# Optimization experiments

Measured on AMD Instinct MI355X. Metric: run time of the kernel, lower is better.

## Reference

```python
import jax, jax.numpy as jnp
import numpy as np

N_NODES = 50000
N_EDGES = 800000
DIM_FEAT = 96
INFO_DIM = 32
DIM_EMB = 160
CONV_OUT = DIM_EMB - INFO_DIM  # 128
NUM_LAYERS = 3
NUM_GRAPHS = 500
DIM_TARGET = 10


def setup_inputs() -> dict:
    key = jax.random.key(0)
    ks = jax.random.split(key, 20)
    inp = {
        'x': jax.random.normal(ks[0], (N_NODES, DIM_FEAT), dtype=jnp.float32),
        'edge_index': jax.random.randint(ks[1], (2, N_EDGES), 0, N_NODES, dtype=jnp.int32),
        'batch': jnp.sort(jax.random.randint(ks[2], (N_NODES,), 0, NUM_GRAPHS, dtype=jnp.int32)),
        'struc_info': jax.random.normal(ks[3], (NUM_GRAPHS, INFO_DIM), dtype=jnp.float32),
    }
    # SAGEConv params per layer: lin_l (on aggregated neighbors, with bias), lin_r (on root, no bias)
    in_dims = [DIM_FEAT + INFO_DIM, DIM_EMB, DIM_EMB]
    k = 4
    for i, din in enumerate(in_dims):
        s = 1.0 / np.sqrt(din)
        inp[f'Wl{i}'] = jax.random.uniform(ks[k], (din, CONV_OUT), jnp.float32, -s, s); k += 1
        inp[f'Wr{i}'] = jax.random.uniform(ks[k], (din, CONV_OUT), jnp.float32, -s, s); k += 1
        inp[f'b{i}'] = jax.random.uniform(ks[k], (CONV_OUT,), jnp.float32, -s, s); k += 1
    s1 = 1.0 / np.sqrt(NUM_LAYERS * CONV_OUT)
    inp['Wfc1'] = jax.random.uniform(ks[k], (NUM_LAYERS * CONV_OUT, DIM_EMB), jnp.float32, -s1, s1); k += 1
    inp['bfc1'] = jax.random.uniform(ks[k], (DIM_EMB,), jnp.float32, -s1, s1); k += 1
    s2 = 1.0 / np.sqrt(DIM_EMB)
    inp['Wfc2'] = jax.random.uniform(ks[k], (DIM_EMB, DIM_TARGET), jnp.float32, -s2, s2); k += 1
    inp['bfc2'] = jax.random.uniform(ks[k], (DIM_TARGET,), jnp.float32, -s2, s2)
    return inp


def _sage_conv(h, src, dst, Wl, Wr, b, n_nodes):
    # PyG SAGEConv (mean aggr): out = lin_l(mean_{j in N(i)} x_j) + lin_r(x_i)
    agg = jax.ops.segment_sum(h[src], dst, num_segments=n_nodes)       # [N, D]
    deg = jax.ops.segment_sum(jnp.ones_like(dst, dtype=h.dtype), dst, num_segments=n_nodes)
    mean = agg / jnp.maximum(deg, 1.0)[:, None]
    return mean @ Wl + b + h @ Wr


def reference(x, edge_index, batch, struc_info, Wl0, Wr0, b0, Wl1, Wr1, b1, Wl2, Wr2, b2, Wfc1, bfc1, Wfc2, bfc2):
    n_nodes = x.shape[0]
    src, dst = edge_index[0], edge_index[1]
    info = struc_info[batch]                         # [N, info_dim] repeated per node
    params = [(Wl0, Wr0, b0), (Wl1, Wr1, b1), (Wl2, Wr2, b2)]
    h = x
    outs = []
    for (Wl, Wr, b) in params:
        h = _sage_conv(jnp.concatenate([h, info], axis=1), src, dst, Wl, Wr, b, n_nodes)
        outs.append(h)
    hcat = jnp.concatenate(outs, axis=1)             # [N, num_layers*conv_out]
    g = jax.ops.segment_max(hcat, batch, num_segments=struc_info.shape[0])  # global max pool
    z = jax.nn.relu(g @ Wfc1 + bfc1)
    return z @ Wfc2 + bfc2
```

## Files before the change

### kernel.cpp

```cpp
#include <hip/hip_runtime.h>
#include <hip/hip_bf16.h>
#include <float.h>

#define NN 50000
#define NE 800000
#define DF 96
#define DI 32
#define CO 128
#define NG 500
#define HC 384
#define F1I 384
#define F1O 160
#define F2O 10
#define CAPLOG 7

typedef unsigned int  u32;
typedef unsigned short u16;
typedef short bf16x8 __attribute__((ext_vector_type(8)));
typedef float f32x4  __attribute__((ext_vector_type(4)));

__device__ __forceinline__ u16 f2b(float f) {
    __hip_bfloat16 h = __float2bfloat16(f);
    return *reinterpret_cast<u16*>(&h);
}
__device__ __forceinline__ float b2f(u16 u) {
    return __uint_as_float(((u32)u) << 16);
}
__device__ __forceinline__ float blo(u32 u) { return __uint_as_float(u << 16); }
__device__ __forceinline__ float bhi(u32 u) { return __uint_as_float(u & 0xffff0000u); }

#define PB_CNT    196
#define PB_STARTS 196
#define PB_CAST   4688
#define PB_WT0    96
#define PB_WT1    128
#define PB_WT2    128
#define PB_INFO   500
#define PREP_GRID (PB_CNT + PB_STARTS + PB_CAST + PB_WT0 + PB_WT1 + PB_WT2 + 3 * PB_INFO)

__global__ __launch_bounds__(256) void k_prep(
        const float* __restrict__ x, const int* __restrict__ batch, const float* __restrict__ info,
        const float* __restrict__ Wl0, const float* __restrict__ Wr0, const float* __restrict__ b0,
        const float* __restrict__ Wl1, const float* __restrict__ Wr1, const float* __restrict__ b1,
        const float* __restrict__ Wl2, const float* __restrict__ Wr2, const float* __restrict__ b2,
        int* __restrict__ cnt, int* __restrict__ start, u16* __restrict__ xb,
        u16* __restrict__ WT0, u16* __restrict__ WT1, u16* __restrict__ WT2,
        float* __restrict__ iQl0, float* __restrict__ iQr0,
        float* __restrict__ iQl1, float* __restrict__ iQr1,
        float* __restrict__ iQl2, float* __restrict__ iQr2) {
    int blk = blockIdx.x;
    int t = threadIdx.x;
    if (blk < PB_CNT) {
        int i = blk * 256 + t;
        if (i < NN) cnt[i] = 0;
        return;
    }
    blk -= PB_CNT;
    if (blk < PB_STARTS) {
        int i = blk * 256 + t;
        if (i >= NN) return;
        int b = batch[i];
        if (i == 0) { for (int g = 0; g <= b; ++g) start[g] = 0; }
        else {
            int p = batch[i - 1];
            if (p != b) for (int g = p + 1; g <= b; ++g) start[g] = i;
        }
        if (i == NN - 1) { for (int g = b + 1; g <= NG; ++g) start[g] = NN; }
        return;
    }
    blk -= PB_STARTS;
    if (blk < PB_CAST) {
        int tid = blk * 256 + t;
        if (tid >= NN * DF / 4) return;
        float4 v = *(const float4*)&x[tid * 4];
        ushort4 o;
        o.x = f2b(v.x); o.y = f2b(v.y); o.z = f2b(v.z); o.w = f2b(v.w);
        *(ushort4*)&xb[tid * 4] = o;
        return;
    }
    blk -= PB_CAST;
    if (blk < PB_WT0 + PB_WT1 + PB_WT2) {
        const float* Wl; const float* Wr; u16* WT; int K; int rel;
        if (blk < PB_WT0) { Wl = Wl0; Wr = Wr0; WT = WT0; K = 96;  rel = blk; }
        else if (blk < PB_WT0 + PB_WT1) { Wl = Wl1; Wr = Wr1; WT = WT1; K = 128; rel = blk - PB_WT0; }
        else { Wl = Wl2; Wr = Wr2; WT = WT2; K = 128; rel = blk - PB_WT0 - PB_WT1; }
        int tid = rel * 256 + t;
        if (tid >= 256 * K) return;
        int n = tid / K;
        int k = tid - n * K;
        float v = (n < CO) ? Wl[k * CO + n] : Wr[k * CO + (n - CO)];
        WT[tid] = f2b(v);
        return;
    }
    blk -= PB_WT0 + PB_WT1 + PB_WT2;
    {
        const float* Wl; const float* Wr; const float* bias; float* iQl; float* iQr; int Ktop; int g;
        if (blk < PB_INFO) { Wl = Wl0; Wr = Wr0; bias = b0; iQl = iQl0; iQr = iQr0; Ktop = 96;  g = blk; }
        else if (blk < 2 * PB_INFO) { Wl = Wl1; Wr = Wr1; bias = b1; iQl = iQl1; iQr = iQr1; Ktop = 128; g = blk - PB_INFO; }
        else { Wl = Wl2; Wr = Wr2; bias = b2; iQl = iQl2; iQr = iQr2; Ktop = 128; g = blk - 2 * PB_INFO; }
        int c = t & 127;
        int sel = t >> 7;
        const float* W = sel ? Wr : Wl;
        float a = sel ? bias[c] : 0.0f;
        for (int d = 0; d < DI; ++d)
            a += info[g * DI + d] * W[(Ktop + d) * CO + c];
        (sel ? iQr : iQl)[g * CO + c] = a;
    }
}

__global__ void k_histfill(const int* __restrict__ src, const int* __restrict__ dst,
                           int* __restrict__ cnt, u16* __restrict__ csr) {
    int e = blockIdx.x * blockDim.x + threadIdx.x;
    if (e >= NE) return;
    int d = dst[e];
    int p = atomicAdd(&cnt[d], 1);
    if (p < (1 << CAPLOG)) csr[(d << CAPLOG) + p] = (u16)src[e];
}

template<int K>
__global__ __launch_bounds__(256) void k_mfma(const u16* __restrict__ A,
                                              const u16* __restrict__ WTg,
                                              const int* __restrict__ batch,
                                              const float* __restrict__ iQl,
                                              const float* __restrict__ iQr,
                                              u16* __restrict__ zlp,
                                              u16* __restrict__ zq) {
    constexpr int PITCH = K + 8;
    __shared__ short lds[256 * PITCH];

    int tid  = threadIdx.x;
    int w    = tid >> 6;
    int lane = tid & 63;
    int quad = lane >> 4;
    int l15  = lane & 15;

    constexpr int CH = 256 * K / 8;
    const uint4* wp = (const uint4*)WTg;
    for (int c = tid; c < CH; c += 256) {
        int n  = c / (K / 8);
        int ko = (c - n * (K / 8)) * 8;
        *(uint4*)&lds[n * PITCH + ko] = wp[c];
    }
    __syncthreads();

    int i0 = blockIdx.x * 128 + w * 32;
    int r0 = i0 + l15;       if (r0 >= NN) r0 = NN - 1;
    int r1 = i0 + 16 + l15;  if (r1 >= NN) r1 = NN - 1;
    const short* A0 = (const short*)A + (size_t)r0 * K;
    const short* A1 = (const short*)A + (size_t)r1 * K;

    f32x4 acc[2][16];
#pragma unroll
    for (int rt = 0; rt < 2; ++rt)
#pragma unroll
        for (int ct = 0; ct < 16; ++ct)
            acc[rt][ct] = (f32x4){0.f, 0.f, 0.f, 0.f};

#pragma unroll
    for (int ks = 0; ks < K / 32; ++ks) {
        int ka = ks * 32 + quad * 8;
        bf16x8 a0 = *(const bf16x8*)(A0 + ka);
        bf16x8 a1 = *(const bf16x8*)(A1 + ka);
#pragma unroll
        for (int ct = 0; ct < 16; ++ct) {
            bf16x8 b = *(const bf16x8*)&lds[(ct * 16 + l15) * PITCH + ka];
            acc[0][ct] = __builtin_amdgcn_mfma_f32_16x16x32_bf16(a0, b, acc[0][ct], 0, 0, 0);
            acc[1][ct] = __builtin_amdgcn_mfma_f32_16x16x32_bf16(a1, b, acc[1][ct], 0, 0, 0);
        }
    }

#pragma unroll
    for (int rt = 0; rt < 2; ++rt) {
#pragma unroll
        for (int reg = 0; reg < 4; ++reg) {
            int row = i0 + rt * 16 + quad * 4 + reg;
            if (row < NN) {
                int b = batch[row];
                const float* ql = &iQl[b * CO];
                const float* qr = &iQr[b * CO];
                u16* lp = zlp + (size_t)row * CO;
                u16* qp = zq  + (size_t)row * CO;
#pragma unroll
                for (int ct = 0; ct < 8; ++ct) {
                    int col = ct * 16 + l15;
                    lp[col] = f2b(acc[rt][ct][reg] + ql[col]);
                }
#pragma unroll
                for (int ct = 8; ct < 16; ++ct) {
                    int col = ct * 16 + l15 - 128;
                    qp[col] = f2b(acc[rt][ct][reg] + qr[col]);
                }
            }
        }
    }
}

__device__ __forceinline__ void acc8(float* a, const uint4& u) {
    a[0] += blo(u.x); a[1] += bhi(u.x);
    a[2] += blo(u.y); a[3] += bhi(u.y);
    a[4] += blo(u.z); a[5] += bhi(u.z);
    a[6] += blo(u.w); a[7] += bhi(u.w);
}

__global__ __launch_bounds__(256) void k_gatherb(const u32* __restrict__ zlp, const u32* __restrict__ zq,
                                                 const int* __restrict__ cnt, const u16* __restrict__ csr,
                                                 u32* __restrict__ hout) {
    int wave = threadIdx.x >> 6;
    int lane = threadIdx.x & 63;
    int q    = lane >> 4;
    int l16  = lane & 15;
    int i = blockIdx.x * 4 + wave;
    if (i >= NN) return;
    int deg = cnt[i];
    int s0 = i << CAPLOG;
    int s1 = s0 + deg;

    const uint4* Z = (const uint4*)zlp;

    float a[8] = {0,0,0,0,0,0,0,0};
    float b[8] = {0,0,0,0,0,0,0,0};
    float c[8] = {0,0,0,0,0,0,0,0};
    float d[8] = {0,0,0,0,0,0,0,0};

    int e = s0;
    for (; e + 15 < s1; e += 16) {
        int n0 = csr[e + q];
        int n1 = csr[e + 4 + q];
        int n2 = csr[e + 8 + q];
        int n3 = csr[e + 12 + q];
        uint4 u0 = Z[(size_t)n0 * 16 + l16];
        uint4 u1 = Z[(size_t)n1 * 16 + l16];
        uint4 u2 = Z[(size_t)n2 * 16 + l16];
        uint4 u3 = Z[(size_t)n3 * 16 + l16];
        acc8(a, u0); acc8(b, u1); acc8(c, u2); acc8(d, u3);
    }
    for (; e < s1; e += 4) {
        if (e + q < s1) {
            int n0 = csr[e + q];
            uint4 u0 = Z[(size_t)n0 * 16 + l16];
            acc8(a, u0);
        }
    }
#pragma unroll
    for (int j = 0; j < 8; ++j) {
        a[j] += b[j] + c[j] + d[j];
        a[j] += __shfl_xor(a[j], 16);
        a[j] += __shfl_xor(a[j], 32);
    }
    if (q == 0) {
        float r = 1.0f / fmaxf((float)deg, 1.0f);
        uint4 qq = ((const uint4*)zq)[(size_t)i * 16 + l16];
        uint4 o;
        o.x = (u32)f2b(a[0] * r + blo(qq.x)) | ((u32)f2b(a[1] * r + bhi(qq.x)) << 16);
        o.y = (u32)f2b(a[2] * r + blo(qq.y)) | ((u32)f2b(a[3] * r + bhi(qq.y)) << 16);
        o.z = (u32)f2b(a[4] * r + blo(qq.z)) | ((u32)f2b(a[5] * r + bhi(qq.z)) << 16);
        o.w = (u32)f2b(a[6] * r + blo(qq.w)) | ((u32)f2b(a[7] * r + bhi(qq.w)) << 16);
        ((uint4*)hout)[(size_t)i * 16 + l16] = o;
    }
}

__global__ __launch_bounds__(384) void k_poolfc(const u16* __restrict__ h1, const u16* __restrict__ h2,
                                                const u16* __restrict__ h3, const int* __restrict__ start,
                                                const float* __restrict__ W1, const float* __restrict__ b1,
                                                const float* __restrict__ W2, const float* __restrict__ b2,
                                                float* __restrict__ out) {
    __shared__ float s_g[F1I];
    __shared__ float s_z[F1O];
    int gr = blockIdx.x;
    int c  = threadIdx.x;
    int sel = c >> 7;
    int cc  = c & 127;
    const u16* hb = (sel == 0) ? h1 : (sel == 1) ? h2 : h3;
    int s = start[gr], e = start[gr + 1];
    float m0 = -FLT_MAX, m1 = -FLT_MAX;
    int n = s;
    for (; n + 1 < e; n += 2) {
        m0 = fmaxf(m0, b2f(hb[n * 128 + cc]));
        m1 = fmaxf(m1, b2f(hb[(n + 1) * 128 + cc]));
    }
    if (n < e) m0 = fmaxf(m0, b2f(hb[n * 128 + cc]));
    s_g[c] = fmaxf(m0, m1);
    __syncthreads();
    if (c < F1O) {
        float acc = b1[c];
        for (int k = 0; k < F1I; ++k) acc += s_g[k] * W1[k * F1O + c];
        s_z[c] = fmaxf(acc, 0.0f);
    }
    __syncthreads();
    if (c < F2O) {
        float a = b2[c];
        for (int k = 0; k < F1O; ++k) a += s_z[k] * W2[k * F2O + c];
        out[gr * F2O + c] = a;
    }
}

extern "C" void kernel_launch(void* const* d_in, const int* in_sizes, int n_in,
                              void* d_out, int out_size, void* d_ws, size_t ws_size,
                              hipStream_t stream) {
    const float* x     = (const float*)d_in[0];
    const int*   eidx  = (const int*)d_in[1];
    const int*   batch = (const int*)d_in[2];
    const float* info  = (const float*)d_in[3];
    const float* Wl0 = (const float*)d_in[4];
    const float* Wr0 = (const float*)d_in[5];
    const float* b0  = (const float*)d_in[6];
    const float* Wl1 = (const float*)d_in[7];
    const float* Wr1 = (const float*)d_in[8];
    const float* b1  = (const float*)d_in[9];
    const float* Wl2 = (const float*)d_in[10];
    const float* Wr2 = (const float*)d_in[11];
    const float* b2  = (const float*)d_in[12];
    const float* Wfc1  = (const float*)d_in[13];
    const float* bfc1  = (const float*)d_in[14];
    const float* Wfc2  = (const float*)d_in[15];
    const float* bfc2  = (const float*)d_in[16];
    float* out = (float*)d_out;

    const int* src = eidx;
    const int* dst = eidx + NE;

    char* W = (char*)d_ws;
    u16* xb     = (u16*)(W + 0);
    u16* h1     = (u16*)(W + 9600000);
    u16* h2     = (u16*)(W + 22400000);
    u16* h3     = (u16*)(W + 35200000);
    u16* zlp    = (u16*)(W + 48000000);
    u16* zq     = (u16*)(W + 60800000);
    u16* WT0    = (u16*)(W + 73600000);
    u16* WT1    = (u16*)(W + 73649152);
    u16* WT2    = (u16*)(W + 73714688);
    float* iQl0 = (float*)(W + 73780224);
    float* iQr0 = (float*)(W + 74036224);
    float* iQl1 = (float*)(W + 74292224);
    float* iQr1 = (float*)(W + 74548224);
    float* iQl2 = (float*)(W + 74804224);
    float* iQr2 = (float*)(W + 75060224);
    int* start  = (int*)(W + 75316224);
    int* cnt    = (int*)(W + 75318272);
    u16* csr    = (u16*)(W + 75518336);

    k_prep<<<PREP_GRID, 256, 0, stream>>>(x, batch, info,
        Wl0, Wr0, b0, Wl1, Wr1, b1, Wl2, Wr2, b2,
        cnt, start, xb, WT0, WT1, WT2, iQl0, iQr0, iQl1, iQr1, iQl2, iQr2);

    k_histfill<<<(NE + 255) / 256, 256, 0, stream>>>(src, dst, cnt, csr);

    const int gGemm = (NN + 127) / 128;
    const int gGath = (NN + 3) / 4;

    k_mfma<96><<<gGemm, 256, 0, stream>>>(xb, WT0, batch, iQl0, iQr0, zlp, zq);
    k_gatherb<<<gGath, 256, 0, stream>>>((const u32*)zlp, (const u32*)zq, cnt, csr, (u32*)h1);

    k_mfma<128><<<gGemm, 256, 0, stream>>>(h1, WT1, batch, iQl1, iQr1, zlp, zq);
    k_gatherb<<<gGath, 256, 0, stream>>>((const u32*)zlp, (const u32*)zq, cnt, csr, (u32*)h2);

    k_mfma<128><<<gGemm, 256, 0, stream>>>(h2, WT2, batch, iQl2, iQr2, zlp, zq);
    k_gatherb<<<gGath, 256, 0, stream>>>((const u32*)zlp, (const u32*)zq, cnt, csr, (u32*)h3);

    k_poolfc<<<NG, 384, 0, stream>>>(h1, h2, h3, start, Wfc1, bfc1, Wfc2, bfc2, out);
}
```

Measured before the change: 332.0 us.

## Fuse edge histogram/CSR fill into prep kernel and widen pooling loads

Moves the atomic histogram and CSR fill into the prep kernel, with each thread handling four edges through vector loads. The counter zeroing becomes a memset issued before the kernel, which removes one launch and lets the edge work overlap with the casting and weight prep. The gather now clamps the degree to the CSR capacity, which fixes reads past a node's slot range. The pooling kernel reads packed bf16 pairs per lane and splits each graph's nodes between two waves, giving more parallelism and fewer loads.

```diff
diff --git a/kernel.cpp b/kernel.cpp
--- a/kernel.cpp
+++ b/kernel.cpp
@@ -29,33 +29,46 @@
 __device__ __forceinline__ float blo(u32 u) { return __uint_as_float(u << 16); }
 __device__ __forceinline__ float bhi(u32 u) { return __uint_as_float(u & 0xffff0000u); }
 
-#define PB_CNT    196
+#define PB_EDGE   782
 #define PB_STARTS 196
 #define PB_CAST   4688
 #define PB_WT0    96
 #define PB_WT1    128
 #define PB_WT2    128
 #define PB_INFO   500
-#define PREP_GRID (PB_CNT + PB_STARTS + PB_CAST + PB_WT0 + PB_WT1 + PB_WT2 + 3 * PB_INFO)
+#define PREP_GRID (PB_EDGE + PB_STARTS + PB_CAST + PB_WT0 + PB_WT1 + PB_WT2 + 3 * PB_INFO)
 
 __global__ __launch_bounds__(256) void k_prep(
         const float* __restrict__ x, const int* __restrict__ batch, const float* __restrict__ info,
+        const int* __restrict__ src, const int* __restrict__ dst,
         const float* __restrict__ Wl0, const float* __restrict__ Wr0, const float* __restrict__ b0,
         const float* __restrict__ Wl1, const float* __restrict__ Wr1, const float* __restrict__ b1,
         const float* __restrict__ Wl2, const float* __restrict__ Wr2, const float* __restrict__ b2,
-        int* __restrict__ cnt, int* __restrict__ start, u16* __restrict__ xb,
+        int* __restrict__ cnt, u16* __restrict__ csr,
+        int* __restrict__ start, u16* __restrict__ xb,
         u16* __restrict__ WT0, u16* __restrict__ WT1, u16* __restrict__ WT2,
         float* __restrict__ iQl0, float* __restrict__ iQr0,
         float* __restrict__ iQl1, float* __restrict__ iQr1,
         float* __restrict__ iQl2, float* __restrict__ iQr2) {
     int blk = blockIdx.x;
     int t = threadIdx.x;
-    if (blk < PB_CNT) {
-        int i = blk * 256 + t;
-        if (i < NN) cnt[i] = 0;
+    if (blk < PB_EDGE) {
+        int base = (blk * 256 + t) * 4;
+        if (base < NE) {
+            int4 dv = *(const int4*)&dst[base];
+            int4 sv = *(const int4*)&src[base];
+            int p0 = atomicAdd(&cnt[dv.x], 1);
+            int p1 = atomicAdd(&cnt[dv.y], 1);
+            int p2 = atomicAdd(&cnt[dv.z], 1);
+            int p3 = atomicAdd(&cnt[dv.w], 1);
+            if (p0 < (1 << CAPLOG)) csr[(dv.x << CAPLOG) + p0] = (u16)sv.x;
+            if (p1 < (1 << CAPLOG)) csr[(dv.y << CAPLOG) + p1] = (u16)sv.y;
+            if (p2 < (1 << CAPLOG)) csr[(dv.z << CAPLOG) + p2] = (u16)sv.z;
+            if (p3 < (1 << CAPLOG)) csr[(dv.w << CAPLOG) + p3] = (u16)sv.w;
+        }
         return;
     }
-    blk -= PB_CNT;
+    blk -= PB_EDGE;
     if (blk < PB_STARTS) {
         int i = blk * 256 + t;
         if (i >= NN) return;
@@ -108,15 +121,6 @@
     }
 }
 
-__global__ void k_histfill(const int* __restrict__ src, const int* __restrict__ dst,
-                           int* __restrict__ cnt, u16* __restrict__ csr) {
-    int e = blockIdx.x * blockDim.x + threadIdx.x;
-    if (e >= NE) return;
-    int d = dst[e];
-    int p = atomicAdd(&cnt[d], 1);
-    if (p < (1 << CAPLOG)) csr[(d << CAPLOG) + p] = (u16)src[e];
-}
-
 template<int K>
 __global__ __launch_bounds__(256) void k_mfma(const u16* __restrict__ A,
                                               const u16* __restrict__ WTg,
@@ -212,8 +216,9 @@
     int i = blockIdx.x * 4 + wave;
     if (i >= NN) return;
     int deg = cnt[i];
+    int degc = min(deg, 1 << CAPLOG);
     int s0 = i << CAPLOG;
-    int s1 = s0 + deg;
+    int s1 = s0 + degc;
 
     const uint4* Z = (const uint4*)zlp;
 
@@ -259,38 +264,64 @@
     }
 }
 
-__global__ __launch_bounds__(384) void k_poolfc(const u16* __restrict__ h1, const u16* __restrict__ h2,
-                                                const u16* __restrict__ h3, const int* __restrict__ start,
+__global__ __launch_bounds__(384) void k_poolfc(const u32* __restrict__ h1, const u32* __restrict__ h2,
+                                                const u32* __restrict__ h3, const int* __restrict__ start,
                                                 const float* __restrict__ W1, const float* __restrict__ b1,
                                                 const float* __restrict__ W2, const float* __restrict__ b2,
                                                 float* __restrict__ out) {
+    __shared__ float s_part[6][128];
     __shared__ float s_g[F1I];
     __shared__ float s_z[F1O];
     int gr = blockIdx.x;
-    int c  = threadIdx.x;
-    int sel = c >> 7;
-    int cc  = c & 127;
-    const u16* hb = (sel == 0) ? h1 : (sel == 1) ? h2 : h3;
+    int t  = threadIdx.x;
+    int w    = t >> 6;
+    int lane = t & 63;
+    int buf  = w % 3;
+    int half = w / 3;
+    const u32* hb = (buf == 0) ? h1 : (buf == 1) ? h2 : h3;
     int s = start[gr], e = start[gr + 1];
-    float m0 = -FLT_MAX, m1 = -FLT_MAX;
-    int n = s;
-    for (; n + 1 < e; n += 2) {
-        m0 = fmaxf(m0, b2f(hb[n * 128 + cc]));
-        m1 = fmaxf(m1, b2f(hb[(n + 1) * 128 + cc]));
-    }
-    if (n < e) m0 = fmaxf(m0, b2f(hb[n * 128 + cc]));
-    s_g[c] = fmaxf(m0, m1);
+    int mid = (s + e) >> 1;
+    int n0 = half ? mid : s;
+    int n1 = half ? e : mid;
+
+    float mlo[4], mhi[4];
+#pragma unroll
+    for (int j = 0; j < 4; ++j) { mlo[j] = -FLT_MAX; mhi[j] = -FLT_MAX; }
+    int n = n0;
+    for (; n + 3 < n1; n += 4) {
+        u32 v0 = hb[(size_t)(n + 0) * 64 + lane];
+        u32 v1 = hb[(size_t)(n + 1) * 64 + lane];
+        u32 v2 = hb[(size_t)(n + 2) * 64 + lane];
+        u32 v3 = hb[(size_t)(n + 3) * 64 + lane];
+        mlo[0] = fmaxf(mlo[0], blo(v0)); mhi[0] = fmaxf(mhi[0], bhi(v0));
+        mlo[1] = fmaxf(mlo[1], blo(v1)); mhi[1] = fmaxf(mhi[1], bhi(v1));
+        mlo[2] = fmaxf(mlo[2], blo(v2)); mhi[2] = fmaxf(mhi[2], bhi(v2));
+        mlo[3] = fmaxf(mlo[3], blo(v3)); mhi[3] = fmaxf(mhi[3], bhi(v3));
+    }
+    for (; n < n1; ++n) {
+        u32 v0 = hb[(size_t)n * 64 + lane];
+        mlo[0] = fmaxf(mlo[0], blo(v0)); mhi[0] = fmaxf(mhi[0], bhi(v0));
+    }
+    float lo = fmaxf(fmaxf(mlo[0], mlo[1]), fmaxf(mlo[2], mlo[3]));
+    float hi = fmaxf(fmaxf(mhi[0], mhi[1]), fmaxf(mhi[2], mhi[3]));
+    s_part[w][2 * lane]     = lo;
+    s_part[w][2 * lane + 1] = hi;
     __syncthreads();
-    if (c < F1O) {
-        float acc = b1[c];
-        for (int k = 0; k < F1I; ++k) acc += s_g[k] * W1[k * F1O + c];
-        s_z[c] = fmaxf(acc, 0.0f);
+    {
+        int buf2 = t >> 7, cc = t & 127;
+        s_g[t] = fmaxf(s_part[buf2][cc], s_part[buf2 + 3][cc]);
     }
     __syncthreads();
-    if (c < F2O) {
-        float a = b2[c];
-        for (int k = 0; k < F1O; ++k) a += s_z[k] * W2[k * F2O + c];
-        out[gr * F2O + c] = a;
+    if (t < F1O) {
+        float acc = b1[t];
+        for (int k = 0; k < F1I; ++k) acc += s_g[k] * W1[k * F1O + t];
+        s_z[t] = fmaxf(acc, 0.0f);
+    }
+    __syncthreads();
+    if (t < F2O) {
+        float a = b2[t];
+        for (int k = 0; k < F1O; ++k) a += s_z[k] * W2[k * F2O + t];
+        out[gr * F2O + t] = a;
     }
 }
 
@@ -339,11 +370,11 @@
     int* cnt    = (int*)(W + 75318272);
     u16* csr    = (u16*)(W + 75518336);
 
-    k_prep<<<PREP_GRID, 256, 0, stream>>>(x, batch, info,
+    hipMemsetAsync(cnt, 0, NN * sizeof(int), stream);
+
+    k_prep<<<PREP_GRID, 256, 0, stream>>>(x, batch, info, src, dst,
         Wl0, Wr0, b0, Wl1, Wr1, b1, Wl2, Wr2, b2,
-        cnt, start, xb, WT0, WT1, WT2, iQl0, iQr0, iQl1, iQr1, iQl2, iQr2);
-
-    k_histfill<<<(NE + 255) / 256, 256, 0, stream>>>(src, dst, cnt, csr);
+        cnt, csr, start, xb, WT0, WT1, WT2, iQl0, iQr0, iQl1, iQr1, iQl2, iQr2);
 
     const int gGemm = (NN + 127) / 128;
     const int gGath = (NN + 3) / 4;
@@ -357,5 +388,6 @@
     k_mfma<128><<<gGemm, 256, 0, stream>>>(h2, WT2, batch, iQl2, iQr2, zlp, zq);
     k_gatherb<<<gGath, 256, 0, stream>>>((const u32*)zlp, (const u32*)zq, cnt, csr, (u32*)h3);
 
-    k_poolfc<<<NG, 384, 0, stream>>>(h1, h2, h3, start, Wfc1, bfc1, Wfc2, bfc2, out);
-}
+    k_poolfc<<<NG, 384, 0, stream>>>((const u32*)h1, (const u32*)h2, (const u32*)h3, start,
+                                     Wfc1, bfc1, Wfc2, bfc2, out);
+}
```

After: 324.0 us. 1.02x faster.
